# Performance work log

Hardware: AMD Instinct MI355X
Metric: run time of the kernel (lower is better)

Reference implementation:

```python
import jax, jax.numpy as jnp
import numpy as np

N_NODES = 65536
N_EDGES = 1048576
IN_DIM = 96
HID = 128
OUT = 2 * HID  # GATv2 out_channels (heads=1, concat)
N_ACT = 20
EDGE_DIM = 3
NEG_SLOPE = 0.2
LN_EPS = 1e-5


def _glorot(key, shape):
    fan_in, fan_out = shape[0], shape[1]
    lim = float(np.sqrt(6.0 / (fan_in + fan_out)))
    return jax.random.uniform(key, shape, jnp.float32, -lim, lim)


def setup_inputs() -> dict:
    key = jax.random.key(0)
    ks = jax.random.split(key, 16)
    inputs = jax.random.normal(ks[0], (N_NODES, IN_DIM), jnp.float32)
    edge_index = jax.random.randint(ks[1], (2, N_EDGES), 0, N_NODES, jnp.int32)
    edge_attr = jax.random.normal(ks[2], (N_EDGES, EDGE_DIM), jnp.float32)
    return {
        "inputs": inputs,
        "edge_index": edge_index,
        "edge_attr": edge_attr,
        # MLP base (n_layers=2, layer_norm=True)
        "W0": _glorot(ks[3], (IN_DIM, HID)), "b0": jnp.zeros((HID,), jnp.float32),
        "g0": jnp.ones((HID,), jnp.float32), "be0": jnp.zeros((HID,), jnp.float32),
        "W1": _glorot(ks[4], (HID, HID)), "b1": jnp.zeros((HID,), jnp.float32),
        "g1": jnp.ones((HID,), jnp.float32), "be1": jnp.zeros((HID,), jnp.float32),
        # GATv2Conv params (heads=1)
        "Wl": _glorot(ks[5], (HID, OUT)), "bl": jnp.zeros((OUT,), jnp.float32),
        "Wr": _glorot(ks[6], (HID, OUT)), "br": jnp.zeros((OUT,), jnp.float32),
        "We": _glorot(ks[7], (EDGE_DIM, OUT)),
        "att": _glorot(ks[8], (OUT, 1))[:, 0],
        "Wres": _glorot(ks[9], (HID, OUT)),
        "gat_bias": jnp.zeros((OUT,), jnp.float32),
        # head: ReLU -> LayerNorm(OUT) -> Linear(OUT, n_actions)
        "g2": jnp.ones((OUT,), jnp.float32), "be2": jnp.zeros((OUT,), jnp.float32),
        "Wq": _glorot(ks[10], (OUT, N_ACT)), "bq": jnp.zeros((N_ACT,), jnp.float32),
    }


def _ln(x, g, b):
    mu = jnp.mean(x, axis=-1, keepdims=True)
    var = jnp.mean(jnp.square(x - mu), axis=-1, keepdims=True)
    return (x - mu) * jax.lax.rsqrt(var + LN_EPS) * g + b


def _gatv2(x, edge_index, edge_attr, Wl, bl, Wr, br, We, att, Wres, gat_bias):
    src, dst = edge_index[0], edge_index[1]
    xl = x @ Wl + bl          # [N, OUT]  (source transform)
    xr = x @ Wr + br          # [N, OUT]  (target transform)
    ef = edge_attr @ We       # [E, OUT]
    m = xl[src] + xr[dst] + ef                      # [E, OUT]
    e = jax.nn.leaky_relu(m, NEG_SLOPE) @ att       # [E]
    # softmax over incoming edges per target node
    e_max = jax.ops.segment_max(e, dst, num_segments=N_NODES)
    ex = jnp.exp(e - e_max[dst])
    denom = jax.ops.segment_sum(ex, dst, num_segments=N_NODES)
    alpha = ex / jnp.where(denom == 0, 1.0, denom)[dst]
    out = jax.ops.segment_sum(alpha[:, None] * xl[src], dst, num_segments=N_NODES)
    return out + x @ Wres + gat_bias


def reference(inputs, edge_index, edge_attr, W0, b0, g0, be0, W1, b1, g1, be1,
              Wl, bl, Wr, br, We, att, Wres, gat_bias, g2, be2, Wq, bq):
    x = _ln(jax.nn.relu(inputs @ W0 + b0), g0, be0)
    x = _ln(jax.nn.relu(x @ W1 + b1), g1, be1)
    h = _gatv2(x, edge_index, edge_attr, Wl, bl, Wr, br, We, att, Wres, gat_bias)
    q = _ln(jax.nn.relu(h), g2, be2) @ Wq + bq
    return q
```

## Files before the change

kernel.cpp:

```cpp
#include <hip/hip_runtime.h>
#include <hip/hip_bf16.h>

#define N_NODES 65536
#define N_EDGES 1048576
#define IN_DIM 96
#define HID 128
#define OUTD 256
#define N_ACT 20

typedef unsigned short u16;
typedef unsigned char u8;
typedef unsigned int u32;
typedef __attribute__((ext_vector_type(8))) short bf16x8;
typedef __attribute__((ext_vector_type(4))) float f32x4;
typedef __attribute__((ext_vector_type(2))) float f32x2;

__device__ __forceinline__ float bf2f(u16 v) { return __uint_as_float(((u32)v) << 16); }
__device__ __forceinline__ u16 f2bf(float f) {
    u32 x = __float_as_uint(f);
    return (u16)((x + 0x7fffu + ((x >> 16) & 1u)) >> 16);
}

__device__ __forceinline__ u8 ftofp8_hw(float f) {
    return (u8)((u32)__builtin_amdgcn_cvt_pk_fp8_f32(f, f, 0, false) & 0xffu);
}

template <int CTRL>
__device__ __forceinline__ float dppadd(float p) {
    return p + __uint_as_float((u32)__builtin_amdgcn_update_dpp(
        0, (int)__float_as_uint(p), CTRL, 0xF, 0xF, true));
}
__device__ __forceinline__ float wave_sum_bcast(float p) {
    p = dppadd<0x111>(p);
    p = dppadd<0x112>(p);
    p = dppadd<0x114>(p);
    p = dppadd<0x118>(p);
    p = dppadd<0x142>(p);
    p = dppadd<0x143>(p);
    return __uint_as_float((u32)__builtin_amdgcn_readlane((int)__float_as_uint(p), 63));
}
__device__ __forceinline__ float red16(float p) {
    p = dppadd<0xB1>(p);
    p = dppadd<0x4E>(p);
    p = dppadd<0x141>(p);
    p = dppadd<0x140>(p);
    return p;
}
__device__ __forceinline__ float red32(float p) {
    p = red16(p);
    p = p + __uint_as_float((u32)__builtin_amdgcn_ds_swizzle(
        (int)__float_as_uint(p), 0x401F));
    return p;
}

__global__ __launch_bounds__(256) void k_prep(
    int* __restrict__ deg,
    const float* __restrict__ Wl, const float* __restrict__ Wr, const float* __restrict__ Wres,
    u16* __restrict__ wt,
    const float* __restrict__ W0, u16* __restrict__ wt0,
    const float* __restrict__ W1, u16* __restrict__ wt1,
    const float* __restrict__ Wq, u16* __restrict__ wqB)
{
    int b = blockIdx.x, t = threadIdx.x;
    if (b < 256) {
        deg[b * 256 + t] = 0;
    } else if (b < 640) {
        int idx = (b - 256) * 256 + t;
        int nn = idx >> 7, k = idx & 127;
        float v;
        if (nn < 256) v = Wl[k * OUTD + nn];
        else if (nn < 512) v = Wr[k * OUTD + (nn - 256)];
        else v = Wres[k * OUTD + (nn - 512)];
        wt[idx] = f2bf(v);
    } else if (b < 688) {
        int idx = (b - 640) * 256 + t;
        int nn = idx / 96, k = idx - nn * 96;
        wt0[idx] = f2bf(W0[k * HID + nn]);
    } else if (b < 752) {
        int idx = (b - 688) * 256 + t;
        int nn = idx >> 7, k = idx & 127;
        wt1[idx] = f2bf(W1[k * HID + nn]);
    } else {
        int idx = (b - 752) * 256 + t;
        int tile = idx >> 12, rem = idx & 4095;
        int kk = rem >> 9, ln = (rem >> 3) & 63, j = idx & 7;
        int k = kk * 32 + (ln >> 4) * 8 + j;
        int q = tile * 16 + (ln & 15);
        wqB[idx] = (q < N_ACT) ? f2bf(Wq[k * N_ACT + q]) : (u16)0;
    }
}

__global__ __launch_bounds__(1024) void k_scan(const int* __restrict__ deg, int* __restrict__ off) {
    __shared__ int part[1024];
    int t = threadIdx.x;
    int base = t * 64;
    const int4* d4 = (const int4*)(deg + base);
    int s = 0;
#pragma unroll
    for (int i = 0; i < 16; i++) { int4 v = d4[i]; s += v.x + v.y + v.z + v.w; }
    part[t] = s;
    __syncthreads();
    for (int o = 1; o < 1024; o <<= 1) {
        int v = (t >= o) ? part[t - o] : 0;
        __syncthreads();
        part[t] += v;
        __syncthreads();
    }
    int run = (t == 0) ? 0 : part[t - 1];
    int4* o4 = (int4*)(off + base);
#pragma unroll
    for (int i = 0; i < 16; i++) {
        int4 v = d4[i];
        int4 w;
        w.x = run;
        w.y = run + v.x;
        w.z = w.y + v.y;
        w.w = w.z + v.z;
        run = w.w + v.w;
        o4[i] = w;
    }
    if (t == 1023) off[N_NODES] = run;
}

__global__ __launch_bounds__(256) void k_scatter(
    const int* __restrict__ ei, const float* __restrict__ ea,
    const int* __restrict__ off, const int* __restrict__ rank,
    int4* __restrict__ erec)
{
    int t4 = blockIdx.x * 256 + threadIdx.x;
    int4 src4 = ((const int4*)ei)[t4];
    int4 dst4 = ((const int4*)(ei + N_EDGES))[t4];
    int4 rk4  = ((const int4*)rank)[t4];
    int o0 = off[dst4.x], o1 = off[dst4.y], o2 = off[dst4.z], o3 = off[dst4.w];
    const float4* ea4 = (const float4*)(ea + (long)t4 * 12);
    float4 a = ea4[0], b = ea4[1], c = ea4[2];
    erec[o0 + rk4.x] = make_int4(src4.x, __float_as_int(a.x), __float_as_int(a.y), __float_as_int(a.z));
    erec[o1 + rk4.y] = make_int4(src4.y, __float_as_int(a.w), __float_as_int(b.x), __float_as_int(b.y));
    erec[o2 + rk4.z] = make_int4(src4.z, __float_as_int(b.z), __float_as_int(b.w), __float_as_int(c.x));
    erec[o3 + rk4.w] = make_int4(src4.w, __float_as_int(c.y), __float_as_int(c.z), __float_as_int(c.w));
}

__global__ __launch_bounds__(256, 4) void k_fused(
    const float* __restrict__ in,
    const u16* __restrict__ wt0, const u16* __restrict__ wt1, const u16* __restrict__ wt,
    const float* __restrict__ b0, const float* __restrict__ g0, const float* __restrict__ be0,
    const float* __restrict__ b1, const float* __restrict__ g1, const float* __restrict__ be1,
    const float* __restrict__ bl, const float* __restrict__ br, const float* __restrict__ gbias,
    const int* __restrict__ ei, int* __restrict__ deg, int* __restrict__ rank,
    u8* __restrict__ xl8, u16* __restrict__ xr, u16* __restrict__ hres)
{
    if (blockIdx.x >= 512) {
        int e = (blockIdx.x - 512) * 256 + threadIdx.x;
        rank[e] = atomicAdd(deg + ei[N_EDGES + e], 1);
        return;
    }
    int wid = threadIdx.x >> 6, lane = threadIdx.x & 63;
    int l15 = lane & 15, quad = lane >> 4;
    int m0 = (blockIdx.x * 4 + wid) * 32;

    __shared__ u16 xbuf[4][32][136];

    f32x4 acc[2][8];

#pragma unroll
    for (int mt = 0; mt < 2; mt++)
#pragma unroll
        for (int t = 0; t < 8; t++) acc[mt][t] = {0.f, 0.f, 0.f, 0.f};
#pragma unroll
    for (int kk = 0; kk < 3; kk++) {
        bf16x8 af[2];
#pragma unroll
        for (int mt = 0; mt < 2; mt++) {
            const float* ap = in + (long)(m0 + mt * 16 + l15) * IN_DIM + kk * 32 + quad * 8;
            float4 fa = *(const float4*)(ap);
            float4 fb = *(const float4*)(ap + 4);
            af[mt][0] = (short)f2bf(fa.x); af[mt][1] = (short)f2bf(fa.y);
            af[mt][2] = (short)f2bf(fa.z); af[mt][3] = (short)f2bf(fa.w);
            af[mt][4] = (short)f2bf(fb.x); af[mt][5] = (short)f2bf(fb.y);
            af[mt][6] = (short)f2bf(fb.z); af[mt][7] = (short)f2bf(fb.w);
        }
#pragma unroll
        for (int t = 0; t < 8; t++) {
            bf16x8 bf = *(const bf16x8*)(wt0 + (t * 16 + l15) * IN_DIM + kk * 32 + quad * 8);
            acc[0][t] = __builtin_amdgcn_mfma_f32_16x16x32_bf16(af[0], bf, acc[0][t], 0, 0, 0);
            acc[1][t] = __builtin_amdgcn_mfma_f32_16x16x32_bf16(af[1], bf, acc[1][t], 0, 0, 0);
        }
    }
    {
        float bv[8], gv[8], bev[8];
#pragma unroll
        for (int t = 0; t < 8; t++) {
            int col = t * 16 + l15;
            bv[t] = b0[col]; gv[t] = g0[col]; bev[t] = be0[col];
        }
#pragma unroll
        for (int mt = 0; mt < 2; mt++) {
#pragma unroll
            for (int g = 0; g < 4; g++) {
                float s_ = 0.f, q_ = 0.f;
#pragma unroll
                for (int t = 0; t < 8; t++) {
                    float x = fmaxf(acc[mt][t][g] + bv[t], 0.f);
                    acc[mt][t][g] = x;
                    s_ += x;
                    q_ = fmaf(x, x, q_);
                }
                s_ = red16(s_);
                q_ = red16(q_);
                float mu = s_ * (1.f / HID);
                float var = q_ * (1.f / HID) - mu * mu;
                float rs = rsqrtf(fmaxf(var, 0.f) + 1e-5f);
#pragma unroll
                for (int t = 0; t < 8; t++) {
                    float y = (acc[mt][t][g] - mu) * rs * gv[t] + bev[t];
                    xbuf[wid][mt * 16 + quad * 4 + g][t * 16 + l15] = f2bf(y);
                }
            }
        }
    }

#pragma unroll
    for (int mt = 0; mt < 2; mt++)
#pragma unroll
        for (int t = 0; t < 8; t++) acc[mt][t] = {0.f, 0.f, 0.f, 0.f};
#pragma unroll
    for (int kk = 0; kk < 4; kk++) {
        bf16x8 af0 = *(const bf16x8*)(&xbuf[wid][l15][kk * 32 + quad * 8]);
        bf16x8 af1 = *(const bf16x8*)(&xbuf[wid][16 + l15][kk * 32 + quad * 8]);
#pragma unroll
        for (int t = 0; t < 8; t++) {
            bf16x8 bf = *(const bf16x8*)(wt1 + (t * 16 + l15) * HID + kk * 32 + quad * 8);
            acc[0][t] = __builtin_amdgcn_mfma_f32_16x16x32_bf16(af0, bf, acc[0][t], 0, 0, 0);
            acc[1][t] = __builtin_amdgcn_mfma_f32_16x16x32_bf16(af1, bf, acc[1][t], 0, 0, 0);
        }
    }
    {
        float bv[8], gv[8], bev[8];
#pragma unroll
        for (int t = 0; t < 8; t++) {
            int col = t * 16 + l15;
            bv[t] = b1[col]; gv[t] = g1[col]; bev[t] = be1[col];
        }
#pragma unroll
        for (int mt = 0; mt < 2; mt++) {
#pragma unroll
            for (int g = 0; g < 4; g++) {
                float s_ = 0.f, q_ = 0.f;
#pragma unroll
                for (int t = 0; t < 8; t++) {
                    float x = fmaxf(acc[mt][t][g] + bv[t], 0.f);
                    acc[mt][t][g] = x;
                    s_ += x;
                    q_ = fmaf(x, x, q_);
                }
                s_ = red16(s_);
                q_ = red16(q_);
                float mu = s_ * (1.f / HID);
                float var = q_ * (1.f / HID) - mu * mu;
                float rs = rsqrtf(fmaxf(var, 0.f) + 1e-5f);
#pragma unroll
                for (int t = 0; t < 8; t++) {
                    float y = (acc[mt][t][g] - mu) * rs * gv[t] + bev[t];
                    xbuf[wid][mt * 16 + quad * 4 + g][t * 16 + l15] = f2bf(y);
                }
            }
        }
    }

    for (int nT = 0; nT < 3; nT++) {
        for (int h = 0; h < 2; h++) {
            f32x4 pacc[2][8];
#pragma unroll
            for (int mt = 0; mt < 2; mt++)
#pragma unroll
                for (int t = 0; t < 8; t++) pacc[mt][t] = {0.f, 0.f, 0.f, 0.f};
#pragma unroll
            for (int kk = 0; kk < 4; kk++) {
                bf16x8 af0 = *(const bf16x8*)(&xbuf[wid][l15][kk * 32 + quad * 8]);
                bf16x8 af1 = *(const bf16x8*)(&xbuf[wid][16 + l15][kk * 32 + quad * 8]);
#pragma unroll
                for (int t = 0; t < 8; t++) {
                    bf16x8 bf = *(const bf16x8*)(wt + (long)(nT * 256 + h * 128 + t * 16 + l15) * HID + kk * 32 + quad * 8);
                    pacc[0][t] = __builtin_amdgcn_mfma_f32_16x16x32_bf16(af0, bf, pacc[0][t], 0, 0, 0);
                    pacc[1][t] = __builtin_amdgcn_mfma_f32_16x16x32_bf16(af1, bf, pacc[1][t], 0, 0, 0);
                }
            }
            if (nT == 0) {
#pragma unroll
                for (int t = 0; t < 8; t++) {
                    int col = h * 128 + t * 16 + l15;
                    float bvv = bl[col];
#pragma unroll
                    for (int mt = 0; mt < 2; mt++)
#pragma unroll
                        for (int g = 0; g < 4; g++) {
                            xl8[(long)(m0 + mt * 16 + quad * 4 + g) * OUTD + col] = ftofp8_hw(pacc[mt][t][g] + bvv);
                        }
                }
            } else {
                const float* bias = (nT == 1) ? br : gbias;
                u16* dst = (nT == 1) ? xr : hres;
#pragma unroll
                for (int t = 0; t < 8; t++) {
                    int col = h * 128 + t * 16 + l15;
                    float bvv = bias[col];
#pragma unroll
                    for (int mt = 0; mt < 2; mt++)
#pragma unroll
                        for (int g = 0; g < 4; g++) {
                            dst[(long)(m0 + mt * 16 + quad * 4 + g) * OUTD + col] = f2bf(pacc[mt][t][g] + bvv);
                        }
                }
            }
        }
    }
}

__global__ __launch_bounds__(256, 4) void k_agg_fused(
    const int* __restrict__ off, const int4* __restrict__ erec,
    const u8* __restrict__ xl8, const u16* __restrict__ xr, const u16* __restrict__ hres,
    const float* __restrict__ We, const float* __restrict__ att,
    const float* __restrict__ g2, const float* __restrict__ be2,
    const u16* __restrict__ wqB, const float* __restrict__ bq,
    float* __restrict__ out)
{
    int wid = threadIdx.x >> 6, lane = threadIdx.x & 63;
    int half = lane >> 5, l31 = lane & 31;
    int n = blockIdx.x * 4 + wid;
    int j0 = l31 * 8;
    __shared__ __align__(16) u16 ylds[4][256];

    const float LOG2E = 1.44269504088896f;

    f32x2 w0_[4], w1_[4], w2_[4], at_[4], xr_[4];
    {
        float4 a0 = *(const float4*)(We + j0);
        float4 a1 = *(const float4*)(We + j0 + 4);
        w0_[0] = {a0.x, a0.y}; w0_[1] = {a0.z, a0.w}; w0_[2] = {a1.x, a1.y}; w0_[3] = {a1.z, a1.w};
        float4 b0v = *(const float4*)(We + OUTD + j0);
        float4 b1v = *(const float4*)(We + OUTD + j0 + 4);
        w1_[0] = {b0v.x, b0v.y}; w1_[1] = {b0v.z, b0v.w}; w1_[2] = {b1v.x, b1v.y}; w1_[3] = {b1v.z, b1v.w};
        float4 c0 = *(const float4*)(We + 2 * OUTD + j0);
        float4 c1 = *(const float4*)(We + 2 * OUTD + j0 + 4);
        w2_[0] = {c0.x, c0.y}; w2_[1] = {c0.z, c0.w}; w2_[2] = {c1.x, c1.y}; w2_[3] = {c1.z, c1.w};
        float4 t0 = *(const float4*)(att + j0);
        float4 t1 = *(const float4*)(att + j0 + 4);
        at_[0] = {t0.x * LOG2E, t0.y * LOG2E}; at_[1] = {t0.z * LOG2E, t0.w * LOG2E};
        at_[2] = {t1.x * LOG2E, t1.y * LOG2E}; at_[3] = {t1.z * LOG2E, t1.w * LOG2E};
        ushort4 xa = *(const ushort4*)(xr + (long)n * OUTD + j0);
        ushort4 xb = *(const ushort4*)(xr + (long)n * OUTD + j0 + 4);
        xr_[0] = {bf2f(xa.x), bf2f(xa.y)}; xr_[1] = {bf2f(xa.z), bf2f(xa.w)};
        xr_[2] = {bf2f(xb.x), bf2f(xb.y)}; xr_[3] = {bf2f(xb.z), bf2f(xb.w)};
    }

    int beg = off[n], end = off[n + 1];
    int cnt = end - beg;

    float s = 0.f;
    f32x2 a_[4] = {{0.f, 0.f}, {0.f, 0.f}, {0.f, 0.f}, {0.f, 0.f}};

    auto edge_logit = [&](const int4& R, const uint2& V,
                          f32x2& d0, f32x2& d1, f32x2& d2, f32x2& d3) -> float {
        d0 = __builtin_amdgcn_cvt_pk_f32_fp8((int)V.x, false);
        d1 = __builtin_amdgcn_cvt_pk_f32_fp8((int)V.x, true);
        d2 = __builtin_amdgcn_cvt_pk_f32_fp8((int)V.y, false);
        d3 = __builtin_amdgcn_cvt_pk_f32_fp8((int)V.y, true);
        float ea0 = __int_as_float(R.y), ea1 = __int_as_float(R.z), ea2 = __int_as_float(R.w);
        f32x2 e0v = {ea0, ea0}, e1v = {ea1, ea1}, e2v = {ea2, ea2};
        f32x2 m0 = d0 + xr_[0], m1 = d1 + xr_[1], m2 = d2 + xr_[2], m3 = d3 + xr_[3];
        m0 = __builtin_elementwise_fma(e0v, w0_[0], m0);
        m1 = __builtin_elementwise_fma(e0v, w0_[1], m1);
        m2 = __builtin_elementwise_fma(e0v, w0_[2], m2);
        m3 = __builtin_elementwise_fma(e0v, w0_[3], m3);
        m0 = __builtin_elementwise_fma(e1v, w1_[0], m0);
        m1 = __builtin_elementwise_fma(e1v, w1_[1], m1);
        m2 = __builtin_elementwise_fma(e1v, w1_[2], m2);
        m3 = __builtin_elementwise_fma(e1v, w1_[3], m3);
        m0 = __builtin_elementwise_fma(e2v, w2_[0], m0);
        m1 = __builtin_elementwise_fma(e2v, w2_[1], m1);
        m2 = __builtin_elementwise_fma(e2v, w2_[2], m2);
        m3 = __builtin_elementwise_fma(e2v, w2_[3], m3);
        m0 = __builtin_elementwise_max(m0, 0.2f * m0);
        m1 = __builtin_elementwise_max(m1, 0.2f * m1);
        m2 = __builtin_elementwise_max(m2, 0.2f * m2);
        m3 = __builtin_elementwise_max(m3, 0.2f * m3);
        f32x2 pv = m0 * at_[0];
        pv = __builtin_elementwise_fma(m1, at_[1], pv);
        pv = __builtin_elementwise_fma(m2, at_[2], pv);
        pv = __builtin_elementwise_fma(m3, at_[3], pv);
        return pv[0] + pv[1];
    };

    if (cnt > 0) {
        const u8* xbase = xl8 + j0;
        auto ix = [&](int k) { return beg + min(k + half, cnt - 1); };
        int4 R0 = erec[ix(0)];
        int4 R1 = erec[ix(2)];
        int4 R2 = erec[ix(4)];
        int4 R3 = erec[ix(6)];
        uint2 V0 = *(const uint2*)(xbase + (long)R0.x * OUTD);
        uint2 V1 = *(const uint2*)(xbase + (long)R1.x * OUTD);
#pragma unroll 1
        for (int i = 0; i < cnt; i += 4) {
            int4 R4 = erec[ix(i + 8)];
            int4 R5 = erec[ix(i + 10)];
            uint2 V2 = *(const uint2*)(xbase + (long)R2.x * OUTD);
            uint2 V3 = *(const uint2*)(xbase + (long)R3.x * OUTD);

            f32x2 dA0, dA1, dA2, dA3, dB0, dB1, dB2, dB3;
            float pA = edge_logit(R0, V0, dA0, dA1, dA2, dA3);
            float pB = edge_logit(R1, V1, dB0, dB1, dB2, dB3);

            pA = red32(pA);
            pB = red32(pB);
            if (i + half >= cnt) pA = -1.0e30f;
            if (i + 2 + half >= cnt) pB = -1.0e30f;

            float eA = __builtin_amdgcn_exp2f(pA);
            float eB = __builtin_amdgcn_exp2f(pB);
            s += eA + eB;

            f32x2 eAv = {eA, eA}, eBv = {eB, eB};
            a_[0] = __builtin_elementwise_fma(eAv, dA0, a_[0]);
            a_[1] = __builtin_elementwise_fma(eAv, dA1, a_[1]);
            a_[2] = __builtin_elementwise_fma(eAv, dA2, a_[2]);
            a_[3] = __builtin_elementwise_fma(eAv, dA3, a_[3]);
            a_[0] = __builtin_elementwise_fma(eBv, dB0, a_[0]);
            a_[1] = __builtin_elementwise_fma(eBv, dB1, a_[1]);
            a_[2] = __builtin_elementwise_fma(eBv, dB2, a_[2]);
            a_[3] = __builtin_elementwise_fma(eBv, dB3, a_[3]);

            R0 = R2; R1 = R3; R2 = R4; R3 = R5;
            V0 = V2; V1 = V3;
        }
        s += __shfl_xor(s, 32);
#pragma unroll
        for (int k = 0; k < 4; k++) {
            a_[k][0] += __shfl_xor(a_[k][0], 32);
            a_[k][1] += __shfl_xor(a_[k][1], 32);
        }
    }

    float inv = (cnt > 0) ? 1.f / s : 0.f;

    ushort4 ha = *(const ushort4*)(hres + (long)n * OUTD + j0);
    ushort4 hb = *(const ushort4*)(hres + (long)n * OUTD + j0 + 4);
    float h[8];
    h[0] = fmaxf(fmaf(a_[0][0], inv, bf2f(ha.x)), 0.f);
    h[1] = fmaxf(fmaf(a_[0][1], inv, bf2f(ha.y)), 0.f);
    h[2] = fmaxf(fmaf(a_[1][0], inv, bf2f(ha.z)), 0.f);
    h[3] = fmaxf(fmaf(a_[1][1], inv, bf2f(ha.w)), 0.f);
    h[4] = fmaxf(fmaf(a_[2][0], inv, bf2f(hb.x)), 0.f);
    h[5] = fmaxf(fmaf(a_[2][1], inv, bf2f(hb.y)), 0.f);
    h[6] = fmaxf(fmaf(a_[3][0], inv, bf2f(hb.z)), 0.f);
    h[7] = fmaxf(fmaf(a_[3][1], inv, bf2f(hb.w)), 0.f);

    float sum = ((h[0] + h[1]) + (h[2] + h[3])) + ((h[4] + h[5]) + (h[6] + h[7]));
    float sq = 0.f;
#pragma unroll
    for (int k = 0; k < 8; k++) sq = fmaf(h[k], h[k], sq);
    sum = wave_sum_bcast(sum);
    sq = wave_sum_bcast(sq);
    float mu = sum * (1.f / (2 * OUTD));
    float var = sq * (1.f / (2 * OUTD)) - mu * mu;
    float rs = rsqrtf(fmaxf(var, 0.f) + 1e-5f);

    {
        int jw = j0 + half * 4;
        float4 gv = *(const float4*)(g2 + jw);
        float4 bv = *(const float4*)(be2 + jw);
        int o0 = half * 4;
        ushort4 yy;
        yy.x = f2bf((h[o0 + 0] - mu) * rs * gv.x + bv.x);
        yy.y = f2bf((h[o0 + 1] - mu) * rs * gv.y + bv.y);
        yy.z = f2bf((h[o0 + 2] - mu) * rs * gv.z + bv.z);
        yy.w = f2bf((h[o0 + 3] - mu) * rs * gv.w + bv.w);
        *(ushort4*)(&ylds[wid][jw]) = yy;
    }
    __syncthreads();

    if (wid < 2) {
        int row = lane & 15, qd = lane >> 4;
        const u16* ab = &ylds[row & 3][qd * 8];
        f32x4 cacc = {0.f, 0.f, 0.f, 0.f};
#pragma unroll
        for (int kk = 0; kk < 8; kk++) {
            bf16x8 afrag = *(const bf16x8*)(ab + kk * 32);
            bf16x8 bfrag = *(const bf16x8*)(wqB + ((((wid << 3) + kk) << 6) + lane) * 8);
            cacc = __builtin_amdgcn_mfma_f32_16x16x32_bf16(afrag, bfrag, cacc, 0, 0, 0);
        }
        if (lane < 16) {
            int q = wid * 16 + lane;
            if (q < N_ACT) {
                float bqv = bq[q];
                long nb = (long)blockIdx.x * 4;
#pragma unroll
                for (int g = 0; g < 4; g++)
                    out[(nb + g) * N_ACT + q] = cacc[g] + bqv;
            }
        }
    }
}

extern "C" void kernel_launch(void* const* d_in, const int* in_sizes, int n_in,
                              void* d_out, int out_size, void* d_ws, size_t ws_size,
                              hipStream_t stream) {
    (void)in_sizes; (void)n_in; (void)out_size; (void)ws_size;
    const float* inp  = (const float*)d_in[0];
    const int*   ei   = (const int*)d_in[1];
    const float* ea   = (const float*)d_in[2];
    const float* W0   = (const float*)d_in[3];
    const float* b0   = (const float*)d_in[4];
    const float* g0   = (const float*)d_in[5];
    const float* be0  = (const float*)d_in[6];
    const float* W1   = (const float*)d_in[7];
    const float* b1   = (const float*)d_in[8];
    const float* g1   = (const float*)d_in[9];
    const float* be1  = (const float*)d_in[10];
    const float* Wl   = (const float*)d_in[11];
    const float* bl   = (const float*)d_in[12];
    const float* Wr   = (const float*)d_in[13];
    const float* br   = (const float*)d_in[14];
    const float* We   = (const float*)d_in[15];
    const float* att  = (const float*)d_in[16];
    const float* Wres = (const float*)d_in[17];
    const float* gbias= (const float*)d_in[18];
    const float* g2   = (const float*)d_in[19];
    const float* be2  = (const float*)d_in[20];
    const float* Wq   = (const float*)d_in[21];
    const float* bq   = (const float*)d_in[22];
    float* out = (float*)d_out;

    char* ws = (char*)d_ws;
    size_t o = 0;
    auto alloc = [&](size_t bytes) -> void* {
        void* p = ws + o;
        o += (bytes + 255) & ~(size_t)255;
        return p;
    };
    u8*    xl8    = (u8*)   alloc((size_t)N_NODES * OUTD);
    u16*   xr     = (u16*)  alloc((size_t)N_NODES * OUTD * 2);
    u16*   hres   = (u16*)  alloc((size_t)N_NODES * OUTD * 2);
    int*   deg    = (int*)  alloc((size_t)N_NODES * 4);
    int*   off    = (int*)  alloc((size_t)(N_NODES + 1) * 4);
    int*   rank   = (int*)  alloc((size_t)N_EDGES * 4);
    int4*  erec   = (int4*) alloc((size_t)N_EDGES * 16);
    u16*   wt     = (u16*)  alloc((size_t)768 * HID * 2);
    u16*   wt0    = (u16*)  alloc((size_t)HID * IN_DIM * 2);
    u16*   wt1    = (u16*)  alloc((size_t)HID * HID * 2);
    u16*   wqB    = (u16*)  alloc((size_t)2 * 8 * 64 * 8 * 2);

    k_prep<<<784, 256, 0, stream>>>(deg, Wl, Wr, Wres, wt, W0, wt0, W1, wt1, Wq, wqB);
    k_fused<<<512 + N_EDGES / 256, 256, 0, stream>>>(inp, wt0, wt1, wt,
        b0, g0, be0, b1, g1, be1, bl, br, gbias, ei, deg, rank, xl8, xr, hres);
    k_scan<<<1, 1024, 0, stream>>>(deg, off);
    k_scatter<<<N_EDGES / 1024, 256, 0, stream>>>(ei, ea, off, rank, erec);
    k_agg_fused<<<N_NODES / 4, 256, 0, stream>>>(off, erec, xl8, xr, hres, We, att, g2, be2, wqB, bq, out);
}
```

Before: 403.5 us.

## Split fused MLP kernel so GAT projections overlap edge scatter

Splits the fused node kernel in two. The first runs the two MLP layers, counts degrees in parallel, and writes the bf16 hidden state to a new workspace buffer. The second reloads that state, computes the Wl/Wr/Wres projections, and runs the CSR edge scatter in extra blocks of the same launch, so the projection GEMMs overlap the scatter that used to be its own kernel. This costs an extra round trip of the hidden activations through global memory.

```diff
diff --git a/kernel.cpp b/kernel.cpp
--- a/kernel.cpp
+++ b/kernel.cpp
@@ -122,32 +122,13 @@
     if (t == 1023) off[N_NODES] = run;
 }
 
-__global__ __launch_bounds__(256) void k_scatter(
-    const int* __restrict__ ei, const float* __restrict__ ea,
-    const int* __restrict__ off, const int* __restrict__ rank,
-    int4* __restrict__ erec)
-{
-    int t4 = blockIdx.x * 256 + threadIdx.x;
-    int4 src4 = ((const int4*)ei)[t4];
-    int4 dst4 = ((const int4*)(ei + N_EDGES))[t4];
-    int4 rk4  = ((const int4*)rank)[t4];
-    int o0 = off[dst4.x], o1 = off[dst4.y], o2 = off[dst4.z], o3 = off[dst4.w];
-    const float4* ea4 = (const float4*)(ea + (long)t4 * 12);
-    float4 a = ea4[0], b = ea4[1], c = ea4[2];
-    erec[o0 + rk4.x] = make_int4(src4.x, __float_as_int(a.x), __float_as_int(a.y), __float_as_int(a.z));
-    erec[o1 + rk4.y] = make_int4(src4.y, __float_as_int(a.w), __float_as_int(b.x), __float_as_int(b.y));
-    erec[o2 + rk4.z] = make_int4(src4.z, __float_as_int(b.z), __float_as_int(b.w), __float_as_int(c.x));
-    erec[o3 + rk4.w] = make_int4(src4.w, __float_as_int(c.y), __float_as_int(c.z), __float_as_int(c.w));
-}
-
-__global__ __launch_bounds__(256, 4) void k_fused(
+__global__ __launch_bounds__(256, 4) void k_fused1(
     const float* __restrict__ in,
-    const u16* __restrict__ wt0, const u16* __restrict__ wt1, const u16* __restrict__ wt,
+    const u16* __restrict__ wt0, const u16* __restrict__ wt1,
     const float* __restrict__ b0, const float* __restrict__ g0, const float* __restrict__ be0,
     const float* __restrict__ b1, const float* __restrict__ g1, const float* __restrict__ be1,
-    const float* __restrict__ bl, const float* __restrict__ br, const float* __restrict__ gbias,
     const int* __restrict__ ei, int* __restrict__ deg, int* __restrict__ rank,
-    u8* __restrict__ xl8, u16* __restrict__ xr, u16* __restrict__ hres)
+    u16* __restrict__ x1)
 {
     if (blockIdx.x >= 512) {
         int e = (blockIdx.x - 512) * 256 + threadIdx.x;
@@ -265,6 +246,49 @@
                 }
             }
         }
+    }
+
+#pragma unroll
+    for (int r = 0; r < 8; r++) {
+        int row = r * 4 + quad;
+        bf16x8 v = *(const bf16x8*)(&xbuf[wid][row][l15 * 8]);
+        *(bf16x8*)(x1 + (long)(m0 + row) * HID + l15 * 8) = v;
+    }
+}
+
+__global__ __launch_bounds__(256, 4) void k_fused2(
+    const u16* __restrict__ x1, const u16* __restrict__ wt,
+    const float* __restrict__ bl, const float* __restrict__ br, const float* __restrict__ gbias,
+    const int* __restrict__ ei, const float* __restrict__ ea,
+    const int* __restrict__ off, const int* __restrict__ rank,
+    int4* __restrict__ erec,
+    u8* __restrict__ xl8, u16* __restrict__ xr, u16* __restrict__ hres)
+{
+    if (blockIdx.x >= 512) {
+        int t4 = (blockIdx.x - 512) * 256 + threadIdx.x;
+        int4 src4 = ((const int4*)ei)[t4];
+        int4 dst4 = ((const int4*)(ei + N_EDGES))[t4];
+        int4 rk4  = ((const int4*)rank)[t4];
+        int o0 = off[dst4.x], o1 = off[dst4.y], o2 = off[dst4.z], o3 = off[dst4.w];
+        const float4* ea4 = (const float4*)(ea + (long)t4 * 12);
+        float4 a = ea4[0], b = ea4[1], c = ea4[2];
+        erec[o0 + rk4.x] = make_int4(src4.x, __float_as_int(a.x), __float_as_int(a.y), __float_as_int(a.z));
+        erec[o1 + rk4.y] = make_int4(src4.y, __float_as_int(a.w), __float_as_int(b.x), __float_as_int(b.y));
+        erec[o2 + rk4.z] = make_int4(src4.z, __float_as_int(b.z), __float_as_int(b.w), __float_as_int(c.x));
+        erec[o3 + rk4.w] = make_int4(src4.w, __float_as_int(c.y), __float_as_int(c.z), __float_as_int(c.w));
+        return;
+    }
+    int wid = threadIdx.x >> 6, lane = threadIdx.x & 63;
+    int l15 = lane & 15, quad = lane >> 4;
+    int m0 = (blockIdx.x * 4 + wid) * 32;
+
+    __shared__ u16 xbuf[4][32][136];
+
+#pragma unroll
+    for (int r = 0; r < 8; r++) {
+        int row = r * 4 + quad;
+        bf16x8 v = *(const bf16x8*)(x1 + (long)(m0 + row) * HID + l15 * 8);
+        *(bf16x8*)(&xbuf[wid][row][l15 * 8]) = v;
     }
 
     for (int nT = 0; nT < 3; nT++) {
@@ -541,6 +565,7 @@
     u8*    xl8    = (u8*)   alloc((size_t)N_NODES * OUTD);
     u16*   xr     = (u16*)  alloc((size_t)N_NODES * OUTD * 2);
     u16*   hres   = (u16*)  alloc((size_t)N_NODES * OUTD * 2);
+    u16*   x1     = (u16*)  alloc((size_t)N_NODES * HID * 2);
     int*   deg    = (int*)  alloc((size_t)N_NODES * 4);
     int*   off    = (int*)  alloc((size_t)(N_NODES + 1) * 4);
     int*   rank   = (int*)  alloc((size_t)N_EDGES * 4);
@@ -551,9 +576,10 @@
     u16*   wqB    = (u16*)  alloc((size_t)2 * 8 * 64 * 8 * 2);
 
     k_prep<<<784, 256, 0, stream>>>(deg, Wl, Wr, Wres, wt, W0, wt0, W1, wt1, Wq, wqB);
-    k_fused<<<512 + N_EDGES / 256, 256, 0, stream>>>(inp, wt0, wt1, wt,
-        b0, g0, be0, b1, g1, be1, bl, br, gbias, ei, deg, rank, xl8, xr, hres);
+    k_fused1<<<512 + N_EDGES / 256, 256, 0, stream>>>(inp, wt0, wt1,
+        b0, g0, be0, b1, g1, be1, ei, deg, rank, x1);
     k_scan<<<1, 1024, 0, stream>>>(deg, off);
-    k_scatter<<<N_EDGES / 1024, 256, 0, stream>>>(ei, ea, off, rank, erec);
+    k_fused2<<<512 + N_EDGES / 1024, 256, 0, stream>>>(x1, wt, bl, br, gbias,
+        ei, ea, off, rank, erec, xl8, xr, hres);
     k_agg_fused<<<N_NODES / 4, 256, 0, stream>>>(off, erec, xl8, xr, hres, We, att, g2, be2, wqB, bq, out);
 }
```

Result: no change. 396.4 us (-1.8%).
